# Kernel optimization log

Hardware: AMD Instinct MI355X
Metric: run time of the kernel (lower is better)

Reference implementation:

```python
import jax, jax.numpy as jnp
import numpy as np

FWD_TRUNCATION = 0.05
EPS_LOG = 1e-20


def setup_inputs() -> dict:
    key = jax.random.key(0)
    k1, k2, k3, k4, k5 = jax.random.split(key, 5)
    B, N, M = 32768, 1024, 64
    samples = jax.random.normal(k1, (B, M), dtype=jnp.float32)
    mask = jax.random.uniform(k2, (B, M), dtype=jnp.float32)
    centroids = jax.random.normal(k3, (N, M), dtype=jnp.float32)
    # sd kept away from 0 to avoid huge 1/sd scaling
    sd = jax.random.uniform(k4, (1, M), dtype=jnp.float32) + 0.5
    log_marginal = jax.random.normal(k5, (1, N), dtype=jnp.float32)
    return {"samples": samples, "mask": mask, "centroids": centroids,
            "sd": sd, "log_marginal": log_marginal}


def _masked_pairwise_sq_distances(A, B, mask):
    # A: [B, M] samples, B: [N, M] centroids, mask: [B, M]
    sq_mask = mask * mask
    mA = mask * A
    A_d = jnp.sum(mA * mA, axis=1, keepdims=True)            # [B, 1]
    B_d = sq_mask @ (B * B).T                                 # [B, N]
    cross = (sq_mask * A) @ B.T                                # [B, N]
    return jax.nn.relu(A_d - 2.0 * cross + B_d)               # [B, N]


def _pdf_truncate(pdf, truncation):
    # discretePdfTruncate: zero out entries below truncation * rowmax, renormalize
    threshold = truncation * jnp.max(pdf, axis=-1, keepdims=True)
    pdf = jax.nn.relu(jnp.sign(pdf - threshold)) * pdf
    return pdf / jnp.sum(pdf, axis=-1, keepdims=True)


def reference(samples, mask, centroids, sd, log_marginal):
    # Mahalanobis: fold 1/sd into the mask (sqMahalanobisDistances)
    m = mask / sd
    dist = _masked_pairwise_sq_distances(samples, centroids, m)  # [B, N]
    log_prior = jax.nn.log_softmax(log_marginal, axis=-1)        # [1, N]
    logits = log_prior - 0.5 * dist                              # [B, N]
    # softmaxWithTemperature (temperature=1) -> truncate -> renormalize
    pdf = jax.nn.softmax(logits, axis=-1)
    pdf = _pdf_truncate(pdf, FWD_TRUNCATION)
    log_pdf = jnp.log(pdf + EPS_LOG)                             # logPdfTruncate
    return pdf, log_pdf
```

## Files before the change

### kernel.cpp

```cpp
#include <hip/hip_runtime.h>
#include <math.h>

#define N_C 1024
#define M_F 64
#define B_R 32768
#define R_B 16
#define LDX 132

typedef short bf16x8 __attribute__((ext_vector_type(8)));
typedef float f32x4 __attribute__((ext_vector_type(4)));

__device__ __forceinline__ short f2bf(float x) {
  unsigned b = __float_as_uint(x);
  b += 0x7fffu + ((b >> 16) & 1u);
  return (short)(b >> 16);
}
__device__ __forceinline__ float bf2f(short h) {
  return __uint_as_float(((unsigned)(unsigned short)h) << 16);
}

__global__ void logprior_kernel(const float* __restrict__ lm, float* __restrict__ lp) {
  __shared__ float red[256];
  const int t = threadIdx.x;
  float v[4];
  float mx = -INFINITY;
#pragma unroll
  for (int i = 0; i < 4; ++i) { v[i] = lm[i * 256 + t]; mx = fmaxf(mx, v[i]); }
  red[t] = mx;
  __syncthreads();
  for (int s = 128; s > 0; s >>= 1) {
    if (t < s) red[t] = fmaxf(red[t], red[t + s]);
    __syncthreads();
  }
  mx = red[0];
  __syncthreads();
  float sum = 0.f;
#pragma unroll
  for (int i = 0; i < 4; ++i) { v[i] -= mx; sum += expf(v[i]); }
  red[t] = sum;
  __syncthreads();
  for (int s = 128; s > 0; s >>= 1) {
    if (t < s) red[t] += red[t + s];
    __syncthreads();
  }
  const float l = logf(red[0]);
#pragma unroll
  for (int i = 0; i < 4; ++i) lp[i * 256 + t] = v[i] - l;
}

__global__ void prep_y(const float* __restrict__ centroids,
                       bf16x8* __restrict__ yh, bf16x8* __restrict__ ym,
                       bf16x8* __restrict__ yl) {
  const int tid = blockIdx.x * 256 + threadIdx.x;
  const int l = tid & 63;
  const int c = (tid >> 6) & 63;
  const int s = tid >> 12;
  const int n = c * 16 + (l & 15);
  const int k0 = s * 32 + (l >> 4) * 8;
  bf16x8 h, mid, lo;
#pragma unroll
  for (int j = 0; j < 8; ++j) {
    const int k = k0 + j;
    float y;
    if (k < 64) {
      y = centroids[n * M_F + k];
    } else {
      const float cc = centroids[n * M_F + (k - 64)];
      y = cc * cc;
    }
    const short hh = f2bf(y);
    const float r1 = y - bf2f(hh);
    const short mm = f2bf(r1);
    const float r2 = r1 - bf2f(mm);
    h[j] = hh;
    mid[j] = mm;
    lo[j] = f2bf(r2);
  }
  const int blob = (s * 64 + c) * 64 + l;
  yh[blob] = h;
  ym[blob] = mid;
  yl[blob] = lo;
}

__global__ __launch_bounds__(256, 3) void rmm_main(
    const float* __restrict__ samples, const float* __restrict__ mask,
    const float* __restrict__ sd, const float* __restrict__ lp_g,
    const bf16x8* __restrict__ yh_g, const bf16x8* __restrict__ ym_g,
    const bf16x8* __restrict__ yl_g, float* __restrict__ out) {
  __shared__ float xs[R_B * LDX];
  __shared__ float lp_s[N_C];
  __shared__ float ad_s[R_B];
  __shared__ float red_s[R_B * 4];

  const int t = threadIdx.x;
  const int b0 = blockIdx.x * R_B;
  const int w = t >> 6;
  const int l = t & 63;
  const int m = l & 15;
  const int q = l >> 4;

  *(float4*)(lp_s + (t << 2)) = *(const float4*)(lp_g + (t << 2));

  {
    const int r = t >> 4;
    const int j4 = (t & 15) << 2;
    const float4 s4 = *(const float4*)(samples + (size_t)(b0 + r) * M_F + j4);
    const float4 m4 = *(const float4*)(mask + (size_t)(b0 + r) * M_F + j4);
    const float4 d4 = *(const float4*)(sd + j4);
    const float sa[4] = {s4.x, s4.y, s4.z, s4.w};
    const float ma[4] = {m4.x, m4.y, m4.z, m4.w};
    const float da[4] = {d4.x, d4.y, d4.z, d4.w};
    float ad = 0.f;
#pragma unroll
    for (int k = 0; k < 4; ++k) {
      const float mm = ma[k] / da[k];
      const float uu = mm * mm;
      const float mA = mm * sa[k];
      ad = fmaf(mA, mA, ad);
      xs[r * LDX + j4 + k] = -2.0f * (uu * sa[k]);
      xs[r * LDX + 64 + j4 + k] = uu;
    }
#pragma unroll
    for (int off = 1; off < 16; off <<= 1) ad += __shfl_xor(ad, off, 64);
    if ((t & 15) == 0) ad_s[r] = ad;
  }

  f32x4 acc[16];
#pragma unroll
  for (int c = 0; c < 16; ++c) acc[c] = (f32x4){0.f, 0.f, 0.f, 0.f};

  __syncthreads();

#pragma unroll 1
  for (int s = 0; s < 4; ++s) {
    const float* xp = &xs[m * LDX + s * 32 + q * 8];
    float av[8];
    *(float4*)&av[0] = *(const float4*)xp;
    *(float4*)&av[4] = *(const float4*)(xp + 4);
    bf16x8 ah, am, al;
#pragma unroll
    for (int j = 0; j < 8; ++j) {
      const short hh = f2bf(av[j]);
      const float r1 = av[j] - bf2f(hh);
      const short mm = f2bf(r1);
      const float r2 = r1 - bf2f(mm);
      ah[j] = hh;
      am[j] = mm;
      al[j] = f2bf(r2);
    }

    const size_t base = (size_t)(s * 64 + w * 16) * 64 + l;
    const bf16x8* yh = yh_g + base;
    const bf16x8* ym = ym_g + base;
    const bf16x8* yl = yl_g + base;

    bf16x8 bh[2], bm[2], bl[2];
#pragma unroll
    for (int p = 0; p < 2; ++p) {
      bh[p] = yh[p * 64];
      bm[p] = ym[p * 64];
      bl[p] = yl[p * 64];
    }

#pragma unroll
    for (int c = 0; c < 16; ++c) {
      const bf16x8 cbh = bh[c & 1];
      const bf16x8 cbm = bm[c & 1];
      const bf16x8 cbl = bl[c & 1];
      if (c + 2 < 16) {
        bh[c & 1] = yh[(c + 2) * 64];
        bm[c & 1] = ym[(c + 2) * 64];
        bl[c & 1] = yl[(c + 2) * 64];
      }
      acc[c] = __builtin_amdgcn_mfma_f32_16x16x32_bf16(am, cbl, acc[c], 0, 0, 0);
      acc[c] = __builtin_amdgcn_mfma_f32_16x16x32_bf16(al, cbm, acc[c], 0, 0, 0);
      acc[c] = __builtin_amdgcn_mfma_f32_16x16x32_bf16(ah, cbl, acc[c], 0, 0, 0);
      acc[c] = __builtin_amdgcn_mfma_f32_16x16x32_bf16(am, cbm, acc[c], 0, 0, 0);
      acc[c] = __builtin_amdgcn_mfma_f32_16x16x32_bf16(al, cbh, acc[c], 0, 0, 0);
      acc[c] = __builtin_amdgcn_mfma_f32_16x16x32_bf16(ah, cbm, acc[c], 0, 0, 0);
      acc[c] = __builtin_amdgcn_mfma_f32_16x16x32_bf16(am, cbh, acc[c], 0, 0, 0);
      acc[c] = __builtin_amdgcn_mfma_f32_16x16x32_bf16(ah, cbh, acc[c], 0, 0, 0);
    }
  }

  float adv[4];
#pragma unroll
  for (int g = 0; g < 4; ++g) adv[g] = ad_s[q * 4 + g];
  float lpv[16];
#pragma unroll
  for (int c = 0; c < 16; ++c) lpv[c] = lp_s[w * 256 + c * 16 + m];

#pragma unroll
  for (int c = 0; c < 16; ++c)
#pragma unroll
    for (int g = 0; g < 4; ++g) {
      const float dist = fmaxf(adv[g] + acc[c][g], 0.0f);
      acc[c][g] = lpv[c] - 0.5f * dist;
    }

  float mx[4];
#pragma unroll
  for (int g = 0; g < 4; ++g) {
    float v = acc[0][g];
#pragma unroll
    for (int c = 1; c < 16; ++c) v = fmaxf(v, acc[c][g]);
#pragma unroll
    for (int off = 1; off < 16; off <<= 1) v = fmaxf(v, __shfl_xor(v, off, 64));
    mx[g] = v;
  }
  if (m == 0) {
#pragma unroll
    for (int g = 0; g < 4; ++g) red_s[(q * 4 + g) * 4 + w] = mx[g];
  }
  __syncthreads();
#pragma unroll
  for (int g = 0; g < 4; ++g) {
    const float4 rv = *(const float4*)(&red_s[(q * 4 + g) * 4]);
    mx[g] = fmaxf(fmaxf(rv.x, rv.y), fmaxf(rv.z, rv.w));
  }
  __syncthreads();

  float sm[4];
#pragma unroll
  for (int g = 0; g < 4; ++g) {
    float ssum = 0.f;
#pragma unroll
    for (int c = 0; c < 16; ++c) {
      const float e = expf(acc[c][g] - mx[g]);
      acc[c][g] = e;
      ssum += e;
    }
#pragma unroll
    for (int off = 1; off < 16; off <<= 1) ssum += __shfl_xor(ssum, off, 64);
    sm[g] = ssum;
  }
  if (m == 0) {
#pragma unroll
    for (int g = 0; g < 4; ++g) red_s[(q * 4 + g) * 4 + w] = sm[g];
  }
  __syncthreads();
#pragma unroll
  for (int g = 0; g < 4; ++g) {
    const float4 rv = *(const float4*)(&red_s[(q * 4 + g) * 4]);
    sm[g] = (rv.x + rv.y) + (rv.z + rv.w);
  }
  __syncthreads();

  float thr[4], qs[4];
#pragma unroll
  for (int g = 0; g < 4; ++g) {
    const float S1 = sm[g];
    thr[g] = 0.05f * (1.0f / S1);
    float s2 = 0.f;
#pragma unroll
    for (int c = 0; c < 16; ++c) {
      const float p = acc[c][g] / S1;
      acc[c][g] = p;
      s2 += (p > thr[g]) ? p : 0.0f;
    }
#pragma unroll
    for (int off = 1; off < 16; off <<= 1) s2 += __shfl_xor(s2, off, 64);
    qs[g] = s2;
  }
  if (m == 0) {
#pragma unroll
    for (int g = 0; g < 4; ++g) red_s[(q * 4 + g) * 4 + w] = qs[g];
  }
  __syncthreads();
#pragma unroll
  for (int g = 0; g < 4; ++g) {
    const float4 rv = *(const float4*)(&red_s[(q * 4 + g) * 4]);
    qs[g] = (rv.x + rv.y) + (rv.z + rv.w);
  }

  const size_t colbase = (size_t)(w * 256 + m);
#pragma unroll
  for (int g = 0; g < 4; ++g) {
    float* orow = out + (size_t)(b0 + q * 4 + g) * N_C + colbase;
    float* lrow = orow + (size_t)B_R * N_C;
#pragma unroll
    for (int c = 0; c < 16; ++c) {
      const float p = acc[c][g];
      const float pf = (p > thr[g]) ? (p / qs[g]) : 0.0f;
      orow[c * 16] = pf;
      lrow[c * 16] = logf(pf + 1e-20f);
    }
  }
}

extern "C" void kernel_launch(void* const* d_in, const int* in_sizes, int n_in,
                              void* d_out, int out_size, void* d_ws, size_t ws_size,
                              hipStream_t stream) {
  const float* samples   = (const float*)d_in[0];
  const float* mask      = (const float*)d_in[1];
  const float* centroids = (const float*)d_in[2];
  const float* sd        = (const float*)d_in[3];
  const float* lm        = (const float*)d_in[4];
  float* out = (float*)d_out;

  char* ws = (char*)d_ws;
  float* lp  = (float*)ws;
  bf16x8* yh = (bf16x8*)(ws + 4096);
  bf16x8* ym = (bf16x8*)(ws + 4096 + 262144);
  bf16x8* yl = (bf16x8*)(ws + 4096 + 2 * 262144);

  logprior_kernel<<<1, 256, 0, stream>>>(lm, lp);
  prep_y<<<64, 256, 0, stream>>>(centroids, yh, ym, yl);
  rmm_main<<<B_R / R_B, 256, 0, stream>>>(samples, mask, sd, lp, yh, ym, yl, out);
}
```

Before: 344.1 us.

## Use 32-row blocks with 8 waves and 2x2 MFMA register tiling

The block grows to 32 sample rows and 512 threads. Each wave now owns 128 centroid columns and two 16-row M-tiles, so every loaded B fragment is reused across two A tiles. This halves the global traffic for centroid fragments per row, and the loop nest interleaves the eight split-bf16 MFMA products across independent accumulators. The cost is more registers per thread and 8-way cross-wave reductions for the softmax statistics, which may lower occupancy.

New measurement: 377.8 us. 9.8% more time.

```diff
diff --git a/kernel.cpp b/kernel.cpp
--- a/kernel.cpp
+++ b/kernel.cpp
@@ -4,7 +4,7 @@
 #define N_C 1024
 #define M_F 64
 #define B_R 32768
-#define R_B 16
+#define R_B 32
 #define LDX 132
 
 typedef short bf16x8 __attribute__((ext_vector_type(8)));
@@ -82,7 +82,7 @@
   yl[blob] = lo;
 }
 
-__global__ __launch_bounds__(256, 3) void rmm_main(
+__global__ __launch_bounds__(512, 2) void rmm_main(
     const float* __restrict__ samples, const float* __restrict__ mask,
     const float* __restrict__ sd, const float* __restrict__ lp_g,
     const bf16x8* __restrict__ yh_g, const bf16x8* __restrict__ ym_g,
@@ -90,7 +90,7 @@
   __shared__ float xs[R_B * LDX];
   __shared__ float lp_s[N_C];
   __shared__ float ad_s[R_B];
-  __shared__ float red_s[R_B * 4];
+  __shared__ float red_s[R_B * 8];
 
   const int t = threadIdx.x;
   const int b0 = blockIdx.x * R_B;
@@ -99,7 +99,7 @@
   const int m = l & 15;
   const int q = l >> 4;
 
-  *(float4*)(lp_s + (t << 2)) = *(const float4*)(lp_g + (t << 2));
+  if (t < 256) *(float4*)(lp_s + (t << 2)) = *(const float4*)(lp_g + (t << 2));
 
   {
     const int r = t >> 4;
@@ -125,167 +125,212 @@
     if ((t & 15) == 0) ad_s[r] = ad;
   }
 
-  f32x4 acc[16];
-#pragma unroll
-  for (int c = 0; c < 16; ++c) acc[c] = (f32x4){0.f, 0.f, 0.f, 0.f};
-
-  __syncthreads();
+  f32x4 acc[2][8];
+#pragma unroll
+  for (int mt = 0; mt < 2; ++mt)
+#pragma unroll
+    for (int c = 0; c < 8; ++c) acc[mt][c] = (f32x4){0.f, 0.f, 0.f, 0.f};
+
+  __syncthreads();
+
+  const int sx[8] = {1, 2, 0, 1, 2, 0, 1, 0};
+  const int sy[8] = {2, 1, 2, 1, 0, 1, 0, 0};
 
 #pragma unroll 1
   for (int s = 0; s < 4; ++s) {
-    const float* xp = &xs[m * LDX + s * 32 + q * 8];
-    float av[8];
-    *(float4*)&av[0] = *(const float4*)xp;
-    *(float4*)&av[4] = *(const float4*)(xp + 4);
-    bf16x8 ah, am, al;
-#pragma unroll
-    for (int j = 0; j < 8; ++j) {
-      const short hh = f2bf(av[j]);
-      const float r1 = av[j] - bf2f(hh);
-      const short mm = f2bf(r1);
-      const float r2 = r1 - bf2f(mm);
-      ah[j] = hh;
-      am[j] = mm;
-      al[j] = f2bf(r2);
-    }
-
-    const size_t base = (size_t)(s * 64 + w * 16) * 64 + l;
-    const bf16x8* yh = yh_g + base;
-    const bf16x8* ym = ym_g + base;
-    const bf16x8* yl = yl_g + base;
-
-    bf16x8 bh[2], bm[2], bl[2];
-#pragma unroll
-    for (int p = 0; p < 2; ++p) {
-      bh[p] = yh[p * 64];
-      bm[p] = ym[p * 64];
-      bl[p] = yl[p * 64];
-    }
-
-#pragma unroll
-    for (int c = 0; c < 16; ++c) {
-      const bf16x8 cbh = bh[c & 1];
-      const bf16x8 cbm = bm[c & 1];
-      const bf16x8 cbl = bl[c & 1];
-      if (c + 2 < 16) {
-        bh[c & 1] = yh[(c + 2) * 64];
-        bm[c & 1] = ym[(c + 2) * 64];
-        bl[c & 1] = yl[(c + 2) * 64];
-      }
-      acc[c] = __builtin_amdgcn_mfma_f32_16x16x32_bf16(am, cbl, acc[c], 0, 0, 0);
-      acc[c] = __builtin_amdgcn_mfma_f32_16x16x32_bf16(al, cbm, acc[c], 0, 0, 0);
-      acc[c] = __builtin_amdgcn_mfma_f32_16x16x32_bf16(ah, cbl, acc[c], 0, 0, 0);
-      acc[c] = __builtin_amdgcn_mfma_f32_16x16x32_bf16(am, cbm, acc[c], 0, 0, 0);
-      acc[c] = __builtin_amdgcn_mfma_f32_16x16x32_bf16(al, cbh, acc[c], 0, 0, 0);
-      acc[c] = __builtin_amdgcn_mfma_f32_16x16x32_bf16(ah, cbm, acc[c], 0, 0, 0);
-      acc[c] = __builtin_amdgcn_mfma_f32_16x16x32_bf16(am, cbh, acc[c], 0, 0, 0);
-      acc[c] = __builtin_amdgcn_mfma_f32_16x16x32_bf16(ah, cbh, acc[c], 0, 0, 0);
-    }
-  }
-
-  float adv[4];
-#pragma unroll
-  for (int g = 0; g < 4; ++g) adv[g] = ad_s[q * 4 + g];
-  float lpv[16];
-#pragma unroll
-  for (int c = 0; c < 16; ++c) lpv[c] = lp_s[w * 256 + c * 16 + m];
-
-#pragma unroll
-  for (int c = 0; c < 16; ++c)
-#pragma unroll
-    for (int g = 0; g < 4; ++g) {
-      const float dist = fmaxf(adv[g] + acc[c][g], 0.0f);
-      acc[c][g] = lpv[c] - 0.5f * dist;
-    }
-
-  float mx[4];
-#pragma unroll
-  for (int g = 0; g < 4; ++g) {
-    float v = acc[0][g];
-#pragma unroll
-    for (int c = 1; c < 16; ++c) v = fmaxf(v, acc[c][g]);
-#pragma unroll
-    for (int off = 1; off < 16; off <<= 1) v = fmaxf(v, __shfl_xor(v, off, 64));
-    mx[g] = v;
-  }
+    const size_t sbase = (size_t)(s * 64 + w * 8) * 64 + l;
+    const bf16x8* yh = yh_g + sbase;
+    const bf16x8* ym = ym_g + sbase;
+    const bf16x8* yl = yl_g + sbase;
+
+    bf16x8 B[3][2][2];
+#pragma unroll
+    for (int tl = 0; tl < 2; ++tl) {
+      B[0][0][tl] = yh[tl * 64];
+      B[1][0][tl] = ym[tl * 64];
+      B[2][0][tl] = yl[tl * 64];
+    }
+
+    bf16x8 A[3][2];
+#pragma unroll
+    for (int mt = 0; mt < 2; ++mt) {
+      const float* xp = &xs[(mt * 16 + m) * LDX + s * 32 + q * 8];
+      float av[8];
+      *(float4*)&av[0] = *(const float4*)xp;
+      *(float4*)&av[4] = *(const float4*)(xp + 4);
+      bf16x8 ah, amd, alo;
+#pragma unroll
+      for (int j = 0; j < 8; ++j) {
+        const short hh = f2bf(av[j]);
+        const float r1 = av[j] - bf2f(hh);
+        const short mm = f2bf(r1);
+        const float r2 = r1 - bf2f(mm);
+        ah[j] = hh;
+        amd[j] = mm;
+        alo[j] = f2bf(r2);
+      }
+      A[0][mt] = ah;
+      A[1][mt] = amd;
+      A[2][mt] = alo;
+    }
+
+#pragma unroll
+    for (int p = 0; p < 4; ++p) {
+      const int cur = p & 1;
+      const int nxt = cur ^ 1;
+      if (p < 3) {
+#pragma unroll
+        for (int tl = 0; tl < 2; ++tl) {
+          B[0][nxt][tl] = yh[(2 * (p + 1) + tl) * 64];
+          B[1][nxt][tl] = ym[(2 * (p + 1) + tl) * 64];
+          B[2][nxt][tl] = yl[(2 * (p + 1) + tl) * 64];
+        }
+      }
+#pragma unroll
+      for (int sp = 0; sp < 8; ++sp)
+#pragma unroll
+        for (int tl = 0; tl < 2; ++tl)
+#pragma unroll
+          for (int mt = 0; mt < 2; ++mt)
+            acc[mt][2 * p + tl] = __builtin_amdgcn_mfma_f32_16x16x32_bf16(
+                A[sx[sp]][mt], B[sy[sp]][cur][tl], acc[mt][2 * p + tl], 0, 0, 0);
+    }
+  }
+
+  float adv[2][4];
+#pragma unroll
+  for (int mt = 0; mt < 2; ++mt)
+#pragma unroll
+    for (int g = 0; g < 4; ++g) adv[mt][g] = ad_s[mt * 16 + q * 4 + g];
+  float lpv[8];
+#pragma unroll
+  for (int c = 0; c < 8; ++c) lpv[c] = lp_s[w * 128 + c * 16 + m];
+
+#pragma unroll
+  for (int mt = 0; mt < 2; ++mt)
+#pragma unroll
+    for (int c = 0; c < 8; ++c)
+#pragma unroll
+      for (int g = 0; g < 4; ++g) {
+        const float dist = fmaxf(adv[mt][g] + acc[mt][c][g], 0.0f);
+        acc[mt][c][g] = lpv[c] - 0.5f * dist;
+      }
+
+  float mx[2][4];
+#pragma unroll
+  for (int mt = 0; mt < 2; ++mt)
+#pragma unroll
+    for (int g = 0; g < 4; ++g) {
+      float v = acc[mt][0][g];
+#pragma unroll
+      for (int c = 1; c < 8; ++c) v = fmaxf(v, acc[mt][c][g]);
+#pragma unroll
+      for (int off = 1; off < 16; off <<= 1) v = fmaxf(v, __shfl_xor(v, off, 64));
+      mx[mt][g] = v;
+    }
   if (m == 0) {
 #pragma unroll
-    for (int g = 0; g < 4; ++g) red_s[(q * 4 + g) * 4 + w] = mx[g];
-  }
-  __syncthreads();
-#pragma unroll
-  for (int g = 0; g < 4; ++g) {
-    const float4 rv = *(const float4*)(&red_s[(q * 4 + g) * 4]);
-    mx[g] = fmaxf(fmaxf(rv.x, rv.y), fmaxf(rv.z, rv.w));
-  }
-  __syncthreads();
-
-  float sm[4];
-#pragma unroll
-  for (int g = 0; g < 4; ++g) {
-    float ssum = 0.f;
-#pragma unroll
-    for (int c = 0; c < 16; ++c) {
-      const float e = expf(acc[c][g] - mx[g]);
-      acc[c][g] = e;
-      ssum += e;
-    }
-#pragma unroll
-    for (int off = 1; off < 16; off <<= 1) ssum += __shfl_xor(ssum, off, 64);
-    sm[g] = ssum;
-  }
+    for (int mt = 0; mt < 2; ++mt)
+#pragma unroll
+      for (int g = 0; g < 4; ++g) red_s[(mt * 16 + q * 4 + g) * 8 + w] = mx[mt][g];
+  }
+  __syncthreads();
+#pragma unroll
+  for (int mt = 0; mt < 2; ++mt)
+#pragma unroll
+    for (int g = 0; g < 4; ++g) {
+      const int row = mt * 16 + q * 4 + g;
+      const float4 r0 = *(const float4*)(&red_s[row * 8]);
+      const float4 r1 = *(const float4*)(&red_s[row * 8 + 4]);
+      mx[mt][g] = fmaxf(fmaxf(fmaxf(r0.x, r0.y), fmaxf(r0.z, r0.w)),
+                        fmaxf(fmaxf(r1.x, r1.y), fmaxf(r1.z, r1.w)));
+    }
+  __syncthreads();
+
+  float sm[2][4];
+#pragma unroll
+  for (int mt = 0; mt < 2; ++mt)
+#pragma unroll
+    for (int g = 0; g < 4; ++g) {
+      float ssum = 0.f;
+#pragma unroll
+      for (int c = 0; c < 8; ++c) {
+        const float e = expf(acc[mt][c][g] - mx[mt][g]);
+        acc[mt][c][g] = e;
+        ssum += e;
+      }
+#pragma unroll
+      for (int off = 1; off < 16; off <<= 1) ssum += __shfl_xor(ssum, off, 64);
+      sm[mt][g] = ssum;
+    }
   if (m == 0) {
 #pragma unroll
-    for (int g = 0; g < 4; ++g) red_s[(q * 4 + g) * 4 + w] = sm[g];
-  }
-  __syncthreads();
-#pragma unroll
-  for (int g = 0; g < 4; ++g) {
-    const float4 rv = *(const float4*)(&red_s[(q * 4 + g) * 4]);
-    sm[g] = (rv.x + rv.y) + (rv.z + rv.w);
-  }
-  __syncthreads();
-
-  float thr[4], qs[4];
-#pragma unroll
-  for (int g = 0; g < 4; ++g) {
-    const float S1 = sm[g];
-    thr[g] = 0.05f * (1.0f / S1);
-    float s2 = 0.f;
-#pragma unroll
-    for (int c = 0; c < 16; ++c) {
-      const float p = acc[c][g] / S1;
-      acc[c][g] = p;
-      s2 += (p > thr[g]) ? p : 0.0f;
-    }
-#pragma unroll
-    for (int off = 1; off < 16; off <<= 1) s2 += __shfl_xor(s2, off, 64);
-    qs[g] = s2;
-  }
+    for (int mt = 0; mt < 2; ++mt)
+#pragma unroll
+      for (int g = 0; g < 4; ++g) red_s[(mt * 16 + q * 4 + g) * 8 + w] = sm[mt][g];
+  }
+  __syncthreads();
+#pragma unroll
+  for (int mt = 0; mt < 2; ++mt)
+#pragma unroll
+    for (int g = 0; g < 4; ++g) {
+      const int row = mt * 16 + q * 4 + g;
+      const float4 r0 = *(const float4*)(&red_s[row * 8]);
+      const float4 r1 = *(const float4*)(&red_s[row * 8 + 4]);
+      sm[mt][g] = ((r0.x + r0.y) + (r0.z + r0.w)) + ((r1.x + r1.y) + (r1.z + r1.w));
+    }
+  __syncthreads();
+
+  float thr[2][4], qs[2][4];
+#pragma unroll
+  for (int mt = 0; mt < 2; ++mt)
+#pragma unroll
+    for (int g = 0; g < 4; ++g) {
+      const float S1 = sm[mt][g];
+      thr[mt][g] = 0.05f * (1.0f / S1);
+      float s2 = 0.f;
+#pragma unroll
+      for (int c = 0; c < 8; ++c) {
+        const float p = acc[mt][c][g] / S1;
+        acc[mt][c][g] = p;
+        s2 += (p > thr[mt][g]) ? p : 0.0f;
+      }
+#pragma unroll
+      for (int off = 1; off < 16; off <<= 1) s2 += __shfl_xor(s2, off, 64);
+      qs[mt][g] = s2;
+    }
   if (m == 0) {
 #pragma unroll
-    for (int g = 0; g < 4; ++g) red_s[(q * 4 + g) * 4 + w] = qs[g];
-  }
-  __syncthreads();
-#pragma unroll
-  for (int g = 0; g < 4; ++g) {
-    const float4 rv = *(const float4*)(&red_s[(q * 4 + g) * 4]);
-    qs[g] = (rv.x + rv.y) + (rv.z + rv.w);
-  }
-
-  const size_t colbase = (size_t)(w * 256 + m);
-#pragma unroll
-  for (int g = 0; g < 4; ++g) {
-    float* orow = out + (size_t)(b0 + q * 4 + g) * N_C + colbase;
-    float* lrow = orow + (size_t)B_R * N_C;
-#pragma unroll
-    for (int c = 0; c < 16; ++c) {
-      const float p = acc[c][g];
-      const float pf = (p > thr[g]) ? (p / qs[g]) : 0.0f;
-      orow[c * 16] = pf;
-      lrow[c * 16] = logf(pf + 1e-20f);
-    }
-  }
+    for (int mt = 0; mt < 2; ++mt)
+#pragma unroll
+      for (int g = 0; g < 4; ++g) red_s[(mt * 16 + q * 4 + g) * 8 + w] = qs[mt][g];
+  }
+  __syncthreads();
+#pragma unroll
+  for (int mt = 0; mt < 2; ++mt)
+#pragma unroll
+    for (int g = 0; g < 4; ++g) {
+      const int row = mt * 16 + q * 4 + g;
+      const float4 r0 = *(const float4*)(&red_s[row * 8]);
+      const float4 r1 = *(const float4*)(&red_s[row * 8 + 4]);
+      qs[mt][g] = ((r0.x + r0.y) + (r0.z + r0.w)) + ((r1.x + r1.y) + (r1.z + r1.w));
+    }
+
+  const size_t colbase = (size_t)(w * 128 + m);
+#pragma unroll
+  for (int mt = 0; mt < 2; ++mt)
+#pragma unroll
+    for (int g = 0; g < 4; ++g) {
+      float* orow = out + (size_t)(b0 + mt * 16 + q * 4 + g) * N_C + colbase;
+      float* lrow = orow + (size_t)B_R * N_C;
+#pragma unroll
+      for (int c = 0; c < 8; ++c) {
+        const float p = acc[mt][c][g];
+        const float pf = (p > thr[mt][g]) ? (p / qs[mt][g]) : 0.0f;
+        orow[c * 16] = pf;
+        lrow[c * 16] = logf(pf + 1e-20f);
+      }
+    }
 }
 
 extern "C" void kernel_launch(void* const* d_in, const int* in_sizes, int n_in,
@@ -306,5 +351,5 @@
 
   logprior_kernel<<<1, 256, 0, stream>>>(lm, lp);
   prep_y<<<64, 256, 0, stream>>>(centroids, yh, ym, yl);
-  rmm_main<<<B_R / R_B, 256, 0, stream>>>(samples, mask, sd, lp, yh, ym, yl, out);
-}
+  rmm_main<<<B_R / R_B, 512, 0, stream>>>(samples, mask, sd, lp, yh, ym, yl, out);
+}
```
